# Optimization experiments

Hardware: AMD Instinct MI355X
Metric: run time of the kernel (lower is better)

## Reference

```python
import jax, jax.numpy as jnp
import numpy as np

B, S, D, H, SE, DE, DFF = 4, 1024, 1024, 16, 77, 768, 4096


def _ln(x, g, b, eps=1e-5):
    mu = jnp.mean(x, axis=-1, keepdims=True)
    var = jnp.mean((x - mu) ** 2, axis=-1, keepdims=True)
    return (x - mu) * jax.lax.rsqrt(var + eps) * g + b


def _split_heads(x, heads):
    b, s, d = x.shape
    return x.reshape(b, s, heads, d // heads).transpose(0, 2, 1, 3)  # b h s hd


def _attn(q, k, v, heads):
    # memory_efficient_attention equivalent: softmax(q k^T * scale) v, per head
    q, k, v = _split_heads(q, heads), _split_heads(k, heads), _split_heads(v, heads)
    scale = q.shape[-1] ** -0.5
    scores = jnp.einsum('bhqd,bhkd->bhqk', q, k) * scale
    probs = jax.nn.softmax(scores, axis=-1)
    o = jnp.einsum('bhqk,bhkd->bhqd', probs, v)
    b, h, s, hd = o.shape
    return o.transpose(0, 2, 1, 3).reshape(b, s, h * hd)


def _geglu_ff(x, w1, b1, w2, b2):
    proj = x @ w1 + b1
    a, gate = jnp.split(proj, 2, axis=-1)
    return (a * jax.nn.gelu(gate)) @ w2 + b2


def _forward(h1, h2, enc, wq, wk, wv, wqc, wo, bo, ln1g, ln1b, ln2g, ln2b,
             w2q, w2k, w2v, w2o, b2o, wff1, bff1, wff2, bff2):
    # norm1
    n1 = _ln(h1, ln1g[0], ln1b[0])
    n2 = _ln(h2, ln1g[1], ln1b[1])
    # dual-stream uni-direction attention (self + cross with swapped K/V)
    q1, k1, v1, q1c = n1 @ wq[0], n1 @ wk[0], n1 @ wv[0], n1 @ wqc[0]
    q2, k2, v2, q2c = n2 @ wq[1], n2 @ wk[1], n2 @ wv[1], n2 @ wqc[1]
    a1 = _attn(q1, k1, v1, H) + _attn(q1c, k2, v2, H)
    a2 = _attn(q2, k2, v2, H) + _attn(q2c, k1, v1, H)
    a1 = a1 @ wo[0] + bo[0]
    a2 = a2 @ wo[1] + bo[1]
    h1 = h1 + a1
    h2 = h2 + a2
    # cross attention to encoder states (attn2)
    n1 = _ln(h1, ln2g[0], ln2b[0])
    n2 = _ln(h2, ln2g[1], ln2b[1])
    c1 = _attn(n1 @ w2q[0], enc @ w2k[0], enc @ w2v[0], H) @ w2o[0] + b2o[0]
    c2 = _attn(n2 @ w2q[1], enc @ w2k[1], enc @ w2v[1], H) @ w2o[1] + b2o[1]
    h1 = h1 + c1
    h2 = h2 + c2
    # feed-forward (GEGLU), applied to norm2 output exactly as in source
    h1 = h1 + _geglu_ff(n1, wff1[0], bff1[0], wff2[0], bff2[0])
    h2 = h2 + _geglu_ff(n2, wff1[1], bff1[1], wff2[1], bff2[1])
    return (h1, h2)


def setup_inputs() -> dict:
    key = jax.random.key(0)
    ks = jax.random.split(key, 16)
    f = lambda k, shp: jax.random.normal(k, shp, jnp.float32) * 0.02
    return {
        'h1': jax.random.normal(ks[0], (B, S, D), jnp.float32),
        'h2': jax.random.normal(ks[1], (B, S, D), jnp.float32),
        'enc': jax.random.normal(ks[2], (B, SE, DE), jnp.float32),
        'wq': f(ks[3], (2, D, D)), 'wk': f(ks[4], (2, D, D)),
        'wv': f(ks[5], (2, D, D)), 'wqc': f(ks[6], (2, D, D)),
        'wo': f(ks[7], (2, D, D)), 'bo': jnp.zeros((2, D), jnp.float32),
        'ln1g': jnp.ones((2, D), jnp.float32), 'ln1b': jnp.zeros((2, D), jnp.float32),
        'ln2g': jnp.ones((2, D), jnp.float32), 'ln2b': jnp.zeros((2, D), jnp.float32),
        'w2q': f(ks[8], (2, D, D)), 'w2k': f(ks[9], (2, DE, D)),
        'w2v': f(ks[10], (2, DE, D)), 'w2o': f(ks[11], (2, D, D)),
        'b2o': jnp.zeros((2, D), jnp.float32),
        'wff1': f(ks[12], (2, D, 2 * DFF)), 'bff1': jnp.zeros((2, 2 * DFF), jnp.float32),
        'wff2': f(ks[13], (2, DFF, D)), 'bff2': jnp.zeros((2, D), jnp.float32),
    }


def reference(h1, h2, enc, wq, wk, wv, wqc, wo, bo, ln1g, ln1b, ln2g, ln2b,
              w2q, w2k, w2v, w2o, b2o, wff1, bff1, wff2, bff2):
    return _forward(h1, h2, enc, wq, wk, wv, wqc, wo, bo, ln1g, ln1b, ln2g, ln2b,
                    w2q, w2k, w2v, w2o, b2o, wff1, bff1, wff2, bff2)
```

## Files before the change

kernel.cpp:

```cpp
#include <hip/hip_runtime.h>

typedef unsigned short u16;
typedef short v8s __attribute__((ext_vector_type(8)));
typedef float v4f __attribute__((ext_vector_type(4)));

__device__ __forceinline__ float bf2f(u16 u) {
  union { unsigned u; float f; } c; c.u = ((unsigned)u) << 16; return c.f;
}
__device__ __forceinline__ u16 f2bf(float x) {
  union { float f; unsigned u; } c; c.f = x;
  unsigned r = c.u + 0x7fffu + ((c.u >> 16) & 1u);
  return (u16)(r >> 16);
}
__device__ __forceinline__ v4f vzero() { v4f z; z[0]=0.f; z[1]=0.f; z[2]=0.f; z[3]=0.f; return z; }
__device__ __forceinline__ v4f mfma16(v8s a, v8s b, v4f c) {
  return __builtin_amdgcn_mfma_f32_16x16x32_bf16(a, b, c, 0, 0, 0);
}
__device__ __forceinline__ void async_lds16(const void* g, void* l) {
  __builtin_amdgcn_global_load_lds((__attribute__((address_space(1))) void*)g,
                                   (__attribute__((address_space(3))) void*)l, 16, 0, 0);
}
__device__ __forceinline__ float gelu_f(float x) {
  return 0.5f * x * (1.f + tanhf(0.7978845608028654f * (x + 0.044715f * x * x * x)));
}

__global__ void detect_k(const unsigned* __restrict__ p, unsigned* __restrict__ flag) {
  if (threadIdx.x == 0) {
    flag[0] = (p[0] == 0x3F803F80u) ? 1u : 0u;
    flag[1] = 0u;
  }
}

__global__ __launch_bounds__(256) void cvt_k(const unsigned* __restrict__ flag,
    const void* __restrict__ src, u16* __restrict__ dst, int n) {
  int i = (blockIdx.x * 256 + threadIdx.x) * 8;
  if (i >= n) return;
  if (*flag) {
    *(uint4*)(dst + i) = *(const uint4*)((const u16*)src + i);
  } else {
    const float* s = (const float*)src + i;
    #pragma unroll
    for (int j = 0; j < 8; ++j) dst[i + j] = f2bf(s[j]);
  }
}

__global__ __launch_bounds__(256) void tr_k(const unsigned* __restrict__ flag,
    const void* __restrict__ in, u16* __restrict__ out, int R, int C, long outZS) {
  __shared__ u16 tile[32][33];
  size_t zin = (size_t)blockIdx.z * R * C;
  size_t zout = (size_t)blockIdx.z * outZS;
  int c0 = blockIdx.x * 32, r0 = blockIdx.y * 32;
  int tx = threadIdx.x & 31, ty = threadIdx.x >> 5;
  unsigned isbf = *flag;
  const u16* inb = (const u16*)in + zin;
  const float* inf = (const float*)in + zin;
  #pragma unroll
  for (int i = ty; i < 32; i += 8) {
    size_t idx = (size_t)(r0 + i) * C + c0 + tx;
    tile[i][tx] = isbf ? inb[idx] : f2bf(inf[idx]);
  }
  __syncthreads();
  out += zout;
  #pragma unroll
  for (int i = ty; i < 32; i += 8) out[(size_t)(c0 + i) * R + r0 + tx] = tile[tx][i];
}

__global__ __launch_bounds__(256) void vtr_k(const u16* __restrict__ in, u16* __restrict__ out) {
  __shared__ u16 tile[32][33];
  int z = blockIdx.z >> 2, b = blockIdx.z & 3;
  const u16* ip = in + (size_t)z * 16777216 + (size_t)b * 4194304 + 2048;
  u16* op = out + (size_t)z * 4194304 + (size_t)b * 1048576;
  int k0 = blockIdx.x * 32, d0 = blockIdx.y * 32;
  int tx = threadIdx.x & 31, ty = threadIdx.x >> 5;
  #pragma unroll
  for (int i = ty; i < 32; i += 8)
    tile[i][tx] = ip[(size_t)(k0 + i) * 4096 + d0 + tx];
  __syncthreads();
  #pragma unroll
  for (int i = ty; i < 32; i += 8)
    op[(size_t)(d0 + i) * 1024 + k0 + tx] = tile[tx][i];
}

__global__ __launch_bounds__(256) void ln_k(const unsigned* __restrict__ flag,
    const void* __restrict__ src0, const void* __restrict__ src1,
    const u16* __restrict__ gw, const u16* __restrict__ bw, u16* __restrict__ out) {
  int z = blockIdx.y;
  const void* src = z ? src1 : src0;
  out += (size_t)z * 4194304; gw += z * 1024; bw += z * 1024;
  int row = blockIdx.x, t = threadIdx.x;
  unsigned isbf = *flag;
  float4 v;
  if (isbf) {
    uint2 d = ((const uint2*)((const u16*)src + (size_t)row * 1024))[t];
    v.x = bf2f((u16)(d.x & 0xffffu)); v.y = bf2f((u16)(d.x >> 16));
    v.z = bf2f((u16)(d.y & 0xffffu)); v.w = bf2f((u16)(d.y >> 16));
  } else {
    v = ((const float4*)((const float*)src + (size_t)row * 1024))[t];
  }
  float s = v.x + v.y + v.z + v.w;
  float s2 = v.x * v.x + v.y * v.y + v.z * v.z + v.w * v.w;
  #pragma unroll
  for (int o = 32; o; o >>= 1) { s += __shfl_down(s, o); s2 += __shfl_down(s2, o); }
  __shared__ float red[8];
  int w = t >> 6;
  if ((t & 63) == 0) { red[w] = s; red[4 + w] = s2; }
  __syncthreads();
  if (t == 0) {
    red[0] = red[0] + red[1] + red[2] + red[3];
    red[4] = red[4] + red[5] + red[6] + red[7];
  }
  __syncthreads();
  float mu = red[0] * (1.f / 1024.f);
  float var = red[4] * (1.f / 1024.f) - mu * mu;
  float rstd = rsqrtf(var + 1e-5f);
  int c = t * 4;
  float xs[4] = { v.x, v.y, v.z, v.w };
  #pragma unroll
  for (int j = 0; j < 4; ++j) {
    float g = bf2f(gw[c + j]), bb = bf2f(bw[c + j]);
    out[(size_t)row * 1024 + c + j] = f2bf((xs[j] - mu) * rstd * g + bb);
  }
}

template<int EPI>
__global__ __launch_bounds__(256, 2) void gemm_bt(
    const u16* __restrict__ A, const u16* __restrict__ Bt,
    int M, int N, int K, int lda, int ldb, int ldc,
    const u16* __restrict__ bias, const u16* aux,
    float* __restrict__ resF, void* __restrict__ outB,
    long zsA, long zsB, long zsC, int zsBias,
    const void* rin0, const void* rin1,
    const unsigned* __restrict__ flagp)
{
  int z = blockIdx.z;
  A += (size_t)z * zsA;
  Bt += (size_t)z * zsB;
  size_t zc = (size_t)z * zsC;
  unsigned isbf = 0;
  if (EPI == 4 || EPI == 5) isbf = *flagp;
  const void* rin = (EPI == 5) ? (z ? rin1 : rin0) : nullptr;
  __shared__ alignas(16) u16 As[128 * 64];
  __shared__ alignas(16) u16 Bs[128 * 64];
  int tid = threadIdx.x;
  int lane = tid & 63, wave = tid >> 6;
  int l15 = lane & 15, l4 = lane >> 4;
  int wm = wave & 1, wn = wave >> 1;
  int m0 = blockIdx.x * 128, n0 = blockIdx.y * 128;
  v4f acc[4][4];
  #pragma unroll
  for (int i = 0; i < 4; ++i)
    #pragma unroll
    for (int j = 0; j < 4; ++j) acc[i][j] = vzero();

  for (int k0 = 0; k0 < K; k0 += 64) {
    #pragma unroll
    for (int it = 0; it < 4; ++it) {
      int sidx = it * 256 + tid;
      int r = sidx >> 3, cs = (sidx & 7) * 8;
      int ra = m0 + r; if (ra > M - 1) ra = M - 1;
      async_lds16(A + (size_t)ra * lda + k0 + cs, As + (size_t)(it * 256 + wave * 64) * 8);
      async_lds16(Bt + (size_t)(n0 + r) * ldb + k0 + cs, Bs + (size_t)(it * 256 + wave * 64) * 8);
    }
    __syncthreads();
    #pragma unroll
    for (int ks = 0; ks < 2; ++ks) {
      v8s af[4], bfr[4];
      #pragma unroll
      for (int i = 0; i < 4; ++i) {
        af[i]  = *(const v8s*)(As + (wm * 64 + i * 16 + l15) * 64 + ks * 32 + l4 * 8);
        bfr[i] = *(const v8s*)(Bs + (wn * 64 + i * 16 + l15) * 64 + ks * 32 + l4 * 8);
      }
      #pragma unroll
      for (int i = 0; i < 4; ++i)
        #pragma unroll
        for (int j = 0; j < 4; ++j)
          acc[i][j] = mfma16(af[i], bfr[j], acc[i][j]);
    }
    __syncthreads();
  }
  #pragma unroll
  for (int mt = 0; mt < 4; ++mt) {
    #pragma unroll
    for (int r = 0; r < 4; ++r) {
      int gr = m0 + wm * 64 + mt * 16 + l4 * 4 + r;
      if (gr >= M) continue;
      size_t ri = (size_t)gr * ldc;
      size_t ro = zc + ri;
      #pragma unroll
      for (int nt = 0; nt < 4; ++nt) {
        int gc = n0 + wn * 64 + nt * 16 + l15;
        float v = acc[mt][nt][r];
        if (bias) v += bf2f(bias[(size_t)z * zsBias + gc]);
        if (EPI == 0) ((u16*)outB)[ro + gc] = f2bf(v);
        else if (EPI == 1) ((u16*)outB)[ro + gc] = f2bf(gelu_f(v));
        else if (EPI == 2) ((u16*)outB)[ro + gc] = f2bf(v * bf2f(aux[ro + gc]));
        else if (EPI == 3) resF[ro + gc] += v;
        else if (EPI == 5) {
          float h = isbf ? bf2f(((const u16*)rin)[ri + gc]) : ((const float*)rin)[ri + gc];
          resF[ro + gc] = h + v;
        } else {
          float o = resF[ro + gc] + v;
          if (isbf) ((u16*)outB)[ro + gc] = f2bf(o);
          else ((float*)outB)[ro + gc] = o;
        }
      }
    }
  }
}

template<int EPI>
__global__ __launch_bounds__(512, 2) void gemm256(
    const u16* __restrict__ A, const u16* __restrict__ Bt,
    int M, int N, int K, int lda, int ldb, int ldc,
    const u16* __restrict__ bias, const u16* aux, void* __restrict__ outB,
    long zsA, long zsB, long zsC, int zsBias)
{
  __shared__ alignas(16) u16 As[4][8192];
  __shared__ alignas(16) u16 Bs[4][8192];
  int z = blockIdx.z;
  A += (size_t)z * zsA;
  Bt += (size_t)z * zsB;
  size_t zc = (size_t)z * zsC;
  int tid = threadIdx.x, lane = tid & 63, wave = tid >> 6;
  int l15 = lane & 15, l4 = lane >> 4;
  int wm = wave >> 2, wn = wave & 3;
  int m0 = blockIdx.x * 256, n0 = blockIdx.y * 256;
  int sa = l4 ^ ((l15 >> 1) & 3);
  int nG = K >> 5;

  v4f acc[8][4];
  #pragma unroll
  for (int i = 0; i < 8; ++i)
    #pragma unroll
    for (int j = 0; j < 4; ++j) acc[i][j] = vzero();

  auto stageA = [&](int g) {
    int sl = g & 3;
    #pragma unroll
    for (int l = 0; l < 2; ++l) {
      int sidx = l * 512 + tid;
      int r = sidx >> 2, c = sidx & 3;
      async_lds16(A + (size_t)(m0 + r) * lda + g * 32 + ((c ^ ((sidx >> 3) & 3)) * 8),
                  As[sl] + (size_t)(l * 512 + wave * 64) * 8);
    }
  };
  auto stageB = [&](int g) {
    int sl = g & 3;
    #pragma unroll
    for (int l = 0; l < 2; ++l) {
      int sidx = l * 512 + tid;
      int r = sidx >> 2, c = sidx & 3;
      async_lds16(Bt + (size_t)(n0 + r) * ldb + g * 32 + ((c ^ ((sidx >> 3) & 3)) * 8),
                  Bs[sl] + (size_t)(l * 512 + wave * 64) * 8);
    }
  };
  auto gate = [&](int cnt) {
    if (cnt >= 2)      asm volatile("s_waitcnt vmcnt(8)" ::: "memory");
    else if (cnt == 1) asm volatile("s_waitcnt vmcnt(4)" ::: "memory");
    else               asm volatile("s_waitcnt vmcnt(0)" ::: "memory");
    __builtin_amdgcn_sched_barrier(0);
  };

  stageA(0); stageB(0);
  if (1 < nG) { stageA(1); stageB(1); }
  if (2 < nG) { stageA(2); stageB(2); }
  gate((1 < nG) + (2 < nG));
  __builtin_amdgcn_s_barrier();

  auto kstep = [&](int t, int s0, int s1) {
    int g0 = 2 * t, g1 = 2 * t + 1;
    const u16* a0 = As[s0]; const u16* b0 = Bs[s0];
    const u16* a1 = As[s1]; const u16* b1 = Bs[s1];
    v8s af[4], bf[4];
    #pragma unroll
    for (int i = 0; i < 4; ++i) {
      af[i] = *(const v8s*)(a0 + ((wm * 128 + i * 16 + l15) * 4 + sa) * 8);
      bf[i] = *(const v8s*)(b0 + ((wn * 64 + i * 16 + l15) * 4 + sa) * 8);
    }
    if (g0 + 3 < nG) stageA(g0 + 3);
    __builtin_amdgcn_s_barrier();
    __builtin_amdgcn_s_setprio(1);
    #pragma unroll
    for (int i = 0; i < 4; ++i)
      #pragma unroll
      for (int j = 0; j < 4; ++j) acc[i][j] = mfma16(af[i], bf[j], acc[i][j]);
    __builtin_amdgcn_s_setprio(0);
    __builtin_amdgcn_s_barrier();
    #pragma unroll
    for (int i = 0; i < 4; ++i)
      af[i] = *(const v8s*)(a0 + ((wm * 128 + 64 + i * 16 + l15) * 4 + sa) * 8);
    if (g0 + 3 < nG) stageB(g0 + 3);
    __builtin_amdgcn_s_barrier();
    __builtin_amdgcn_s_setprio(1);
    #pragma unroll
    for (int i = 0; i < 4; ++i)
      #pragma unroll
      for (int j = 0; j < 4; ++j) acc[4 + i][j] = mfma16(af[i], bf[j], acc[4 + i][j]);
    __builtin_amdgcn_s_setprio(0);
    gate((g0 + 2 < nG) + (g0 + 3 < nG));
    __builtin_amdgcn_s_barrier();
    #pragma unroll
    for (int i = 0; i < 4; ++i) {
      af[i] = *(const v8s*)(a1 + ((wm * 128 + i * 16 + l15) * 4 + sa) * 8);
      bf[i] = *(const v8s*)(b1 + ((wn * 64 + i * 16 + l15) * 4 + sa) * 8);
    }
    if (g1 + 3 < nG) stageA(g1 + 3);
    __builtin_amdgcn_s_barrier();
    __builtin_amdgcn_s_setprio(1);
    #pragma unroll
    for (int i = 0; i < 4; ++i)
      #pragma unroll
      for (int j = 0; j < 4; ++j) acc[i][j] = mfma16(af[i], bf[j], acc[i][j]);
    __builtin_amdgcn_s_setprio(0);
    __builtin_amdgcn_s_barrier();
    #pragma unroll
    for (int i = 0; i < 4; ++i)
      af[i] = *(const v8s*)(a1 + ((wm * 128 + 64 + i * 16 + l15) * 4 + sa) * 8);
    if (g1 + 3 < nG) stageB(g1 + 3);
    __builtin_amdgcn_s_barrier();
    __builtin_amdgcn_s_setprio(1);
    #pragma unroll
    for (int i = 0; i < 4; ++i)
      #pragma unroll
      for (int j = 0; j < 4; ++j) acc[4 + i][j] = mfma16(af[i], bf[j], acc[4 + i][j]);
    __builtin_amdgcn_s_setprio(0);
    gate((g1 + 2 < nG) + (g1 + 3 < nG));
    __builtin_amdgcn_s_barrier();
  };

  int Ksteps = K >> 6;
  for (int t = 0; t < Ksteps; t += 2) {
    kstep(t, 0, 1);
    kstep(t + 1, 2, 3);
  }

  #pragma unroll
  for (int mi = 0; mi < 8; ++mi) {
    #pragma unroll
    for (int rr = 0; rr < 4; ++rr) {
      int gr = m0 + wm * 128 + mi * 16 + l4 * 4 + rr;
      size_t ro = zc + (size_t)gr * ldc;
      #pragma unroll
      for (int ni = 0; ni < 4; ++ni) {
        int gc = n0 + wn * 64 + ni * 16 + l15;
        float v = acc[mi][ni][rr];
        if (bias) v += bf2f(bias[(size_t)z * zsBias + gc]);
        if (EPI == 0) ((u16*)outB)[ro + gc] = f2bf(v);
        else if (EPI == 1) ((u16*)outB)[ro + gc] = f2bf(gelu_f(v));
        else ((u16*)outB)[ro + gc] = f2bf(v * bf2f(aux[ro + gc]));
      }
    }
  }
}

__global__ __launch_bounds__(256, 2) void flash_self_k(
    const u16* __restrict__ qkv, const u16* __restrict__ Vt, u16* __restrict__ O)
{
  __shared__ alignas(16) u16 Ksh[128 * 64];
  __shared__ alignas(16) u16 Vsh[64 * 128];
  __shared__ alignas(16) u16 Psh[4][16 * 128];
  int tid = threadIdx.x, lane = tid & 63, wave = tid >> 6;
  int l15 = lane & 15, l4 = lane >> 4;
  int h = blockIdx.y;
  int strm = blockIdx.z >> 2, b = blockIdx.z & 3;
  const size_t ZS = 16777216;
  const size_t BS = 4194304;
  int q0 = blockIdx.x * 64 + wave * 16;
  u16* pw = Psh[wave];
  int swz = l15 & 7;
  v4f res[4];
  #pragma unroll
  for (int i = 0; i < 4; ++i) res[i] = vzero();

  for (int sg = 0; sg < 2; ++sg) {
    int qcol = sg ? 3072 : 0;
    int ksrc = sg ? (strm ^ 1) : strm;
    const u16* Qb = qkv + (size_t)strm * ZS + (size_t)b * BS + qcol + h * 64;
    const u16* Kb = qkv + (size_t)ksrc * ZS + (size_t)b * BS + 1024 + h * 64;
    const u16* Vb = Vt + (size_t)ksrc * BS + (size_t)b * 1048576 + h * 65536;
    v8s qf0 = *(const v8s*)(Qb + (size_t)(q0 + l15) * 4096 + l4 * 8);
    v8s qf1 = *(const v8s*)(Qb + (size_t)(q0 + l15) * 4096 + l4 * 8 + 32);
    v4f oacc[4];
    #pragma unroll
    for (int i = 0; i < 4; ++i) oacc[i] = vzero();
    float mrun[4], lrun[4];
    #pragma unroll
    for (int r = 0; r < 4; ++r) { mrun[r] = -1e30f; lrun[r] = 0.f; }

    for (int c0 = 0; c0 < 1024; c0 += 128) {
      #pragma unroll
      for (int it = 0; it < 4; ++it) {
        int sidx = it * 256 + tid;
        int r = sidx >> 3, c = sidx & 7;
        async_lds16(Kb + (size_t)(c0 + r) * 4096 + ((c ^ (r & 7)) * 8),
                    Ksh + (size_t)(it * 256 + wave * 64) * 8);
      }
      #pragma unroll
      for (int it = 0; it < 4; ++it) {
        int sidx = it * 256 + tid;
        int d = sidx >> 4, c = sidx & 15;
        async_lds16(Vb + (size_t)d * 1024 + c0 + ((c ^ (d & 15)) * 8),
                    Vsh + (size_t)(it * 256 + wave * 64) * 8);
      }
      __syncthreads();
      v4f s[4][2];
      #pragma unroll
      for (int g = 0; g < 4; ++g) { s[g][0] = vzero(); s[g][1] = vzero(); }
      __builtin_amdgcn_s_setprio(1);
      #pragma unroll
      for (int g = 0; g < 4; ++g) {
        int rb0 = (g * 32 + l15) * 64, rb1 = rb0 + 16 * 64;
        v8s k00 = *(const v8s*)(Ksh + rb0 + ((l4 ^ swz) * 8));
        v8s k10 = *(const v8s*)(Ksh + rb1 + ((l4 ^ swz) * 8));
        v8s k01 = *(const v8s*)(Ksh + rb0 + (((4 + l4) ^ swz) * 8));
        v8s k11 = *(const v8s*)(Ksh + rb1 + (((4 + l4) ^ swz) * 8));
        s[g][0] = mfma16(qf0, k00, s[g][0]);
        s[g][1] = mfma16(qf0, k10, s[g][1]);
        s[g][0] = mfma16(qf1, k01, s[g][0]);
        s[g][1] = mfma16(qf1, k11, s[g][1]);
      }
      __builtin_amdgcn_s_setprio(0);
      float alpha[4];
      #pragma unroll
      for (int r = 0; r < 4; ++r) {
        int row = l4 * 4 + r;
        float x[8];
        #pragma unroll
        for (int g = 0; g < 4; ++g) {
          x[2 * g]     = s[g][0][r] * 0.125f;
          x[2 * g + 1] = s[g][1][r] * 0.125f;
        }
        float tm = fmaxf(fmaxf(fmaxf(x[0], x[1]), fmaxf(x[2], x[3])),
                         fmaxf(fmaxf(x[4], x[5]), fmaxf(x[6], x[7])));
        #pragma unroll
        for (int o = 8; o; o >>= 1) tm = fmaxf(tm, __shfl_xor(tm, o));
        float mn = fmaxf(mrun[r], tm);
        alpha[r] = __expf(mrun[r] - mn);
        mrun[r] = mn;
        float rs = 0.f;
        #pragma unroll
        for (int j = 0; j < 8; ++j) {
          float p = __expf(x[j] - mn);
          rs += p;
          int col = (j >> 1) * 32 + (j & 1) * 16 + l15;
          pw[row * 128 + (((col >> 3) ^ row) * 8) + (col & 7)] = f2bf(p);
        }
        #pragma unroll
        for (int o = 8; o; o >>= 1) rs += __shfl_xor(rs, o);
        lrun[r] = lrun[r] * alpha[r] + rs;
      }
      #pragma unroll
      for (int nt = 0; nt < 4; ++nt)
        #pragma unroll
        for (int r = 0; r < 4; ++r) oacc[nt][r] *= alpha[r];
      __builtin_amdgcn_s_setprio(1);
      #pragma unroll
      for (int g = 0; g < 4; ++g) {
        v8s pa = *(const v8s*)(pw + l15 * 128 + (((g * 4 + l4) ^ l15) * 8));
        #pragma unroll
        for (int nt = 0; nt < 4; ++nt) {
          int vr = nt * 16 + l15;
          v8s vb = *(const v8s*)(Vsh + vr * 128 + (((g * 4 + l4) ^ (vr & 15)) * 8));
          oacc[nt] = mfma16(pa, vb, oacc[nt]);
        }
      }
      __builtin_amdgcn_s_setprio(0);
      __syncthreads();
    }
    #pragma unroll
    for (int r = 0; r < 4; ++r) {
      float inv = 1.f / lrun[r];
      #pragma unroll
      for (int nt = 0; nt < 4; ++nt) res[nt][r] += oacc[nt][r] * inv;
    }
  }
  #pragma unroll
  for (int nt = 0; nt < 4; ++nt) {
    #pragma unroll
    for (int r = 0; r < 4; ++r) {
      int gq = q0 + l4 * 4 + r;
      size_t oi = (size_t)strm * BS + ((size_t)b * 1024 + gq) * 1024 + h * 64 + nt * 16 + l15;
      O[oi] = f2bf(res[nt][r]);
    }
  }
}

__global__ __launch_bounds__(256, 2) void flash_cross_k(
    const u16* __restrict__ Q, const u16* __restrict__ KV, u16* __restrict__ O)
{
  __shared__ alignas(16) u16 Ksh[128 * 64];
  __shared__ alignas(16) unsigned VshT[64 * 68];
  __shared__ alignas(16) u16 Psh[4][16 * 128];
  int tid = threadIdx.x, lane = tid & 63, wave = tid >> 6;
  int l15 = lane & 15, l4 = lane >> 4;
  int h = blockIdx.y;
  int strm = blockIdx.z >> 2, b = blockIdx.z & 3;
  const u16* Qb = Q + (size_t)strm * 4194304 + (size_t)b * 1048576 + h * 64;
  const u16* Kb = KV + (size_t)strm * 630784 + (size_t)b * 157696 + h * 64;
  const u16* Vb = Kb + 1024;
  int q0 = blockIdx.x * 64 + wave * 16;
  u16* pw = Psh[wave];
  int swz = l15 & 7;
  v8s qf0 = *(const v8s*)(Qb + (size_t)(q0 + l15) * 1024 + l4 * 8);
  v8s qf1 = *(const v8s*)(Qb + (size_t)(q0 + l15) * 1024 + l4 * 8 + 32);

  #pragma unroll
  for (int it = 0; it < 4; ++it) {
    int sidx = it * 256 + tid;
    int r = sidx >> 3, c = sidx & 7;
    int gk = r > 76 ? 76 : r;
    async_lds16(Kb + (size_t)gk * 2048 + ((c ^ (r & 7)) * 8),
                Ksh + (size_t)(it * 256 + wave * 64) * 8);
  }
  #pragma unroll
  for (int it = 0; it < 2; ++it) {
    int tt = it * 256 + tid;
    int kp = tt & 63, dsg = tt >> 6;
    int gk0 = kp * 2, gk1 = kp * 2 + 1;
    if (gk0 > 76) gk0 = 76;
    if (gk1 > 76) gk1 = 76;
    v8s v0 = *(const v8s*)(Vb + (size_t)gk0 * 2048 + dsg * 8);
    v8s v1 = *(const v8s*)(Vb + (size_t)gk1 * 2048 + dsg * 8);
    #pragma unroll
    for (int j = 0; j < 8; ++j) {
      unsigned pk = (unsigned)(u16)v0[j] | ((unsigned)(u16)v1[j] << 16);
      VshT[(dsg * 8 + j) * 68 + kp] = pk;
    }
  }
  __syncthreads();
  v4f s[4][2];
  #pragma unroll
  for (int g = 0; g < 4; ++g) { s[g][0] = vzero(); s[g][1] = vzero(); }
  __builtin_amdgcn_s_setprio(1);
  #pragma unroll
  for (int g = 0; g < 4; ++g) {
    int rb0 = (g * 32 + l15) * 64, rb1 = rb0 + 16 * 64;
    v8s k00 = *(const v8s*)(Ksh + rb0 + ((l4 ^ swz) * 8));
    v8s k10 = *(const v8s*)(Ksh + rb1 + ((l4 ^ swz) * 8));
    v8s k01 = *(const v8s*)(Ksh + rb0 + (((4 + l4) ^ swz) * 8));
    v8s k11 = *(const v8s*)(Ksh + rb1 + (((4 + l4) ^ swz) * 8));
    s[g][0] = mfma16(qf0, k00, s[g][0]);
    s[g][1] = mfma16(qf0, k10, s[g][1]);
    s[g][0] = mfma16(qf1, k01, s[g][0]);
    s[g][1] = mfma16(qf1, k11, s[g][1]);
  }
  __builtin_amdgcn_s_setprio(0);
  float lsum[4];
  #pragma unroll
  for (int r = 0; r < 4; ++r) {
    int row = l4 * 4 + r;
    float x[8];
    #pragma unroll
    for (int g = 0; g < 4; ++g) {
      bool ok0 = (g * 32 + l15) < 77, ok1 = (g * 32 + 16 + l15) < 77;
      x[2 * g]     = ok0 ? s[g][0][r] * 0.125f : -1e30f;
      x[2 * g + 1] = ok1 ? s[g][1][r] * 0.125f : -1e30f;
    }
    float tm = fmaxf(fmaxf(fmaxf(x[0], x[1]), fmaxf(x[2], x[3])),
                     fmaxf(fmaxf(x[4], x[5]), fmaxf(x[6], x[7])));
    #pragma unroll
    for (int o = 8; o; o >>= 1) tm = fmaxf(tm, __shfl_xor(tm, o));
    float rs = 0.f;
    #pragma unroll
    for (int j = 0; j < 8; ++j) {
      float p = __expf(x[j] - tm);
      rs += p;
      int col = (j >> 1) * 32 + (j & 1) * 16 + l15;
      pw[row * 128 + (((col >> 3) ^ row) * 8) + (col & 7)] = f2bf(p);
    }
    #pragma unroll
    for (int o = 8; o; o >>= 1) rs += __shfl_xor(rs, o);
    lsum[r] = rs;
  }
  v4f oacc[4];
  #pragma unroll
  for (int i = 0; i < 4; ++i) oacc[i] = vzero();
  __builtin_amdgcn_s_setprio(1);
  #pragma unroll
  for (int g = 0; g < 4; ++g) {
    v8s pa = *(const v8s*)(pw + l15 * 128 + (((g * 4 + l4) ^ l15) * 8));
    #pragma unroll
    for (int nt = 0; nt < 4; ++nt) {
      v8s vb = *(const v8s*)((const u16*)VshT + (nt * 16 + l15) * 136 + g * 32 + l4 * 8);
      oacc[nt] = mfma16(pa, vb, oacc[nt]);
    }
  }
  __builtin_amdgcn_s_setprio(0);
  #pragma unroll
  for (int nt = 0; nt < 4; ++nt) {
    #pragma unroll
    for (int r = 0; r < 4; ++r) {
      int gq = q0 + l4 * 4 + r;
      size_t oi = (size_t)strm * 4194304 + ((size_t)b * 1024 + gq) * 1024 + h * 64 + nt * 16 + l15;
      O[oi] = f2bf(oacc[nt][r] / lsum[r]);
    }
  }
}

extern "C" void kernel_launch(void* const* d_in, const int* in_sizes, int n_in,
                              void* d_out, int out_size, void* d_ws, size_t ws_size,
                              hipStream_t stream)
{
  (void)in_sizes; (void)n_in; (void)out_size;
  const void* h1   = d_in[0];
  const void* h2   = d_in[1];
  const void* enc  = d_in[2];
  const void* wq   = d_in[3];
  const void* wk   = d_in[4];
  const void* wv   = d_in[5];
  const void* wqc  = d_in[6];
  const void* wo   = d_in[7];
  const void* bo   = d_in[8];
  const void* ln1g = d_in[9];
  const void* ln1b = d_in[10];
  const void* ln2g = d_in[11];
  const void* ln2b = d_in[12];
  const void* w2q  = d_in[13];
  const void* w2k  = d_in[14];
  const void* w2v  = d_in[15];
  const void* w2o  = d_in[16];
  const void* b2o  = d_in[17];
  const void* wff1 = d_in[18];
  const void* bff1 = d_in[19];
  const void* wff2 = d_in[20];
  const void* bff2 = d_in[21];

  const size_t S1 = 4194304;
  const size_t W1 = 1048576;
  const size_t QS = 16777216;
  const size_t NE = 236544;

  char* base = (char*)d_ws;
  size_t off = 0;
  auto AL = [&](size_t n) { size_t r = off; off += (n + 255) & ~(size_t)255; return r; };
  size_t o_flag   = AL(256);
  size_t o_pb     = AL(30720 * 2);
  size_t o_encB   = AL(NE * 2);
  size_t o_wqkvT  = AL(2 * 4 * W1 * 2);
  size_t o_woT    = AL(2 * W1 * 2);
  size_t o_w2qT   = AL(2 * W1 * 2);
  size_t o_w2oT   = AL(2 * W1 * 2);
  size_t o_w2kvT  = AL(2 * 2048 * 768 * 2);
  size_t o_wff1T  = AL(2 * 8192 * 1024 * 2);
  size_t o_wff2T  = AL(2 * 4096 * 1024 * 2);
  size_t o_hw     = AL(2 * S1 * 4);
  size_t o_n      = AL(2 * S1 * 2);
  size_t o_qkv    = AL(2 * QS * 2);
  size_t o_ab     = AL(2 * S1 * 2);
  if (ws_size < off) return;

  unsigned* flagp = (unsigned*)(base + o_flag);
  const unsigned* zerop = flagp + 1;
  u16* pb = (u16*)(base + o_pb);
  u16* boB   = pb + 0;
  u16* b2oB  = pb + 2048;
  u16* ln1gB = pb + 4096;
  u16* ln1bB = pb + 6144;
  u16* ln2gB = pb + 8192;
  u16* ln2bB = pb + 10240;
  u16* bff2B = pb + 12288;
  u16* bff1B = pb + 14336;
  u16* encB  = (u16*)(base + o_encB);
  u16* wqkvT = (u16*)(base + o_wqkvT);
  u16* woT   = (u16*)(base + o_woT);
  u16* w2qT  = (u16*)(base + o_w2qT);
  u16* w2oT  = (u16*)(base + o_w2oT);
  u16* w2kvT = (u16*)(base + o_w2kvT);
  u16* wff1T = (u16*)(base + o_wff1T);
  u16* wff2T = (u16*)(base + o_wff2T);
  float* hw  = (float*)(base + o_hw);
  u16* n1    = (u16*)(base + o_n);
  u16* qkv   = (u16*)(base + o_qkv);
  u16* a1b   = (u16*)(base + o_ab);
  u16* q1x   = qkv;
  u16* c1b   = qkv + 2 * S1;
  u16* kencv = qkv + 4 * S1;
  u16* gelu  = qkv;
  u16* vtb   = n1;

  auto tr = [&](const void* ip, u16* op, int R, int C, long outZS) {
    dim3 g(C / 32, R / 32, 2);
    tr_k<<<g, 256, 0, stream>>>(flagp, ip, op, R, C, outZS);
  };
  auto cvt = [&](const void* ip, u16* op, int n) {
    cvt_k<<<(n / 8 + 255) / 256, 256, 0, stream>>>(flagp, ip, op, n);
  };
  auto gemm = [&](int epi, const u16* Ap, const u16* Bp, int M, int N, int K,
                  int lda, int ldb, int ldc, const u16* bias, const u16* aux,
                  float* resF, void* oB, int nz, long zsA, long zsB, long zsC, int zsBias,
                  const void* rin0, const void* rin1) {
    dim3 g((M + 127) / 128, N / 128, nz);
    switch (epi) {
      case 0: gemm_bt<0><<<g, 256, 0, stream>>>(Ap, Bp, M, N, K, lda, ldb, ldc, bias, aux, resF, oB, zsA, zsB, zsC, zsBias, rin0, rin1, flagp); break;
      case 1: gemm_bt<1><<<g, 256, 0, stream>>>(Ap, Bp, M, N, K, lda, ldb, ldc, bias, aux, resF, oB, zsA, zsB, zsC, zsBias, rin0, rin1, flagp); break;
      case 2: gemm_bt<2><<<g, 256, 0, stream>>>(Ap, Bp, M, N, K, lda, ldb, ldc, bias, aux, resF, oB, zsA, zsB, zsC, zsBias, rin0, rin1, flagp); break;
      case 3: gemm_bt<3><<<g, 256, 0, stream>>>(Ap, Bp, M, N, K, lda, ldb, ldc, bias, aux, resF, oB, zsA, zsB, zsC, zsBias, rin0, rin1, flagp); break;
      case 4: gemm_bt<4><<<g, 256, 0, stream>>>(Ap, Bp, M, N, K, lda, ldb, ldc, bias, aux, resF, oB, zsA, zsB, zsC, zsBias, rin0, rin1, flagp); break;
      default: gemm_bt<5><<<g, 256, 0, stream>>>(Ap, Bp, M, N, K, lda, ldb, ldc, bias, aux, resF, oB, zsA, zsB, zsC, zsBias, rin0, rin1, flagp); break;
    }
  };

  detect_k<<<1, 64, 0, stream>>>((const unsigned*)ln1g, flagp);
  cvt(bo, boB, 2048);     cvt(b2o, b2oB, 2048);
  cvt(ln1g, ln1gB, 2048); cvt(ln1b, ln1bB, 2048);
  cvt(ln2g, ln2gB, 2048); cvt(ln2b, ln2bB, 2048);
  cvt(bff2, bff2B, 2048); cvt(bff1, bff1B, 16384);
  cvt(enc, encB, (int)NE);
  tr(wq,  wqkvT + 0 * W1, 1024, 1024, 4 * (long)W1);
  tr(wk,  wqkvT + 1 * W1, 1024, 1024, 4 * (long)W1);
  tr(wv,  wqkvT + 2 * W1, 1024, 1024, 4 * (long)W1);
  tr(wqc, wqkvT + 3 * W1, 1024, 1024, 4 * (long)W1);
  tr(wo,  woT,  1024, 1024, (long)W1);
  tr(w2q, w2qT, 1024, 1024, (long)W1);
  tr(w2o, w2oT, 1024, 1024, (long)W1);
  tr(w2k, w2kvT + 0,          768, 1024, 2048L * 768);
  tr(w2v, w2kvT + 1024 * 768, 768, 1024, 2048L * 768);
  tr(wff1, wff1T, 1024, 8192, 8192L * 1024);
  tr(wff2, wff2T, 4096, 1024, 4096L * 1024);
  ln_k<<<dim3(4096, 2), 256, 0, stream>>>(flagp, h1, h2, ln1gB, ln1bB, n1);
  gemm256<0><<<dim3(16, 16, 2), 512, 0, stream>>>(n1, wqkvT, 4096, 4096, 1024,
      1024, 1024, 4096, nullptr, nullptr, qkv, (long)S1, 4 * (long)W1, (long)QS, 0);
  vtr_k<<<dim3(32, 32, 8), 256, 0, stream>>>(qkv, vtb);
  flash_self_k<<<dim3(16, 16, 8), 256, 0, stream>>>(qkv, vtb, a1b);
  gemm(5, a1b, woT, 4096, 1024, 1024, 1024, 1024, 1024, boB, nullptr, hw, nullptr,
       2, (long)S1, (long)W1, (long)S1, 1024, h1, h2);
  ln_k<<<dim3(4096, 2), 256, 0, stream>>>(zerop, hw, hw + S1, ln2gB, ln2bB, n1);
  gemm(0, n1, w2qT, 4096, 1024, 1024, 1024, 1024, 1024, nullptr, nullptr, nullptr, q1x,
       2, (long)S1, (long)W1, (long)S1, 0, nullptr, nullptr);
  gemm(0, encB, w2kvT, 308, 2048, 768, 768, 768, 2048, nullptr, nullptr, nullptr, kencv,
       2, 0, 2048L * 768, 308L * 2048, 0, nullptr, nullptr);
  flash_cross_k<<<dim3(16, 16, 8), 256, 0, stream>>>(q1x, kencv, c1b);
  gemm(3, c1b, w2oT, 4096, 1024, 1024, 1024, 1024, 1024, b2oB, nullptr, hw, nullptr,
       2, (long)S1, (long)W1, (long)S1, 1024, nullptr, nullptr);
  gemm256<1><<<dim3(16, 16, 2), 512, 0, stream>>>(n1, wff1T + 4096 * 1024, 4096, 4096, 1024,
      1024, 1024, 4096, bff1B + 4096, nullptr, gelu, (long)S1, 8192L * 1024, (long)QS, 8192);
  gemm256<2><<<dim3(16, 16, 2), 512, 0, stream>>>(n1, wff1T, 4096, 4096, 1024,
      1024, 1024, 4096, bff1B, gelu, gelu, (long)S1, 8192L * 1024, (long)QS, 8192);
  gemm(4, gelu, wff2T, 4096, 1024, 4096, 4096, 4096, 1024,
       bff2B, nullptr, hw, d_out, 2, (long)QS, 4096L * 1024, (long)S1, 1024,
       nullptr, nullptr);
}
```

Measured before the change: 1.199 ms.

## Keep softmax probabilities in registers, skip rescales, swizzle block order

The self-attention kernel now computes S transposed (K as the A operand), so each lane owns one query's scores. That lets it pack the probabilities to bf16 in registers with v_cvt_pk_bf16_f32 and feed them straight into the PV MFMA, removing the per-wave LDS P buffer and its round trip. Online-softmax max rescaling is skipped unless the max grows by more than a threshold, and occupancy is raised to 4 blocks per CU. Both GEMMs and the flash kernel also remap block indices for L2 locality, and the V transpose permutes key columns to match the new P register layout. These changes cut LDS traffic, shuffles and exp work, at the cost of subtle layout coupling and higher register pressure.

```diff
diff --git a/kernel.cpp b/kernel.cpp
--- a/kernel.cpp
+++ b/kernel.cpp
@@ -19,6 +19,11 @@
 __device__ __forceinline__ void async_lds16(const void* g, void* l) {
   __builtin_amdgcn_global_load_lds((__attribute__((address_space(1))) void*)g,
                                    (__attribute__((address_space(3))) void*)l, 16, 0, 0);
+}
+__device__ __forceinline__ unsigned cvtpk(float lo, float hi) {
+  unsigned r;
+  asm("v_cvt_pk_bf16_f32 %0, %1, %2" : "=v"(r) : "v"(lo), "v"(hi));
+  return r;
 }
 __device__ __forceinline__ float gelu_f(float x) {
   return 0.5f * x * (1.f + tanhf(0.7978845608028654f * (x + 0.044715f * x * x * x)));
@@ -76,9 +81,10 @@
   for (int i = ty; i < 32; i += 8)
     tile[i][tx] = ip[(size_t)(k0 + i) * 4096 + d0 + tx];
   __syncthreads();
+  int sl = (((tx >> 3) & 1) << 4) | (((tx >> 2) & 1) << 3) | (((tx >> 4) & 1) << 2) | (tx & 3);
   #pragma unroll
   for (int i = ty; i < 32; i += 8)
-    op[(size_t)(d0 + i) * 1024 + k0 + tx] = tile[tx][i];
+    op[(size_t)(d0 + i) * 1024 + k0 + sl] = tile[tx][i];
 }
 
 __global__ __launch_bounds__(256) void ln_k(const unsigned* __restrict__ flag,
@@ -145,7 +151,11 @@
   int lane = tid & 63, wave = tid >> 6;
   int l15 = lane & 15, l4 = lane >> 4;
   int wm = wave & 1, wn = wave >> 1;
-  int m0 = blockIdx.x * 128, n0 = blockIdx.y * 128;
+  int lin = blockIdx.x + blockIdx.y * gridDim.x;
+  int nxy = gridDim.x * gridDim.y;
+  int sw = (lin & 7) * (nxy >> 3) + (lin >> 3);
+  int bx = sw % gridDim.x, by = sw / gridDim.x;
+  int m0 = bx * 128, n0 = by * 128;
   v4f acc[4][4];
   #pragma unroll
   for (int i = 0; i < 4; ++i)
@@ -224,7 +234,11 @@
   int tid = threadIdx.x, lane = tid & 63, wave = tid >> 6;
   int l15 = lane & 15, l4 = lane >> 4;
   int wm = wave >> 2, wn = wave & 3;
-  int m0 = blockIdx.x * 256, n0 = blockIdx.y * 256;
+  int lin = blockIdx.x + blockIdx.y * gridDim.x;
+  int nxy = gridDim.x * gridDim.y;
+  int sw = (lin & 7) * (nxy >> 3) + (lin >> 3);
+  int bx = sw % gridDim.x, by = sw / gridDim.x;
+  int m0 = bx * 256, n0 = by * 256;
   int sa = l4 ^ ((l15 >> 1) & 3);
   int nG = K >> 5;
 
@@ -353,20 +367,20 @@
   }
 }
 
-__global__ __launch_bounds__(256, 2) void flash_self_k(
+__global__ __launch_bounds__(256, 4) void flash_self_k(
     const u16* __restrict__ qkv, const u16* __restrict__ Vt, u16* __restrict__ O)
 {
   __shared__ alignas(16) u16 Ksh[128 * 64];
   __shared__ alignas(16) u16 Vsh[64 * 128];
-  __shared__ alignas(16) u16 Psh[4][16 * 128];
   int tid = threadIdx.x, lane = tid & 63, wave = tid >> 6;
-  int l15 = lane & 15, l4 = lane >> 4;
-  int h = blockIdx.y;
-  int strm = blockIdx.z >> 2, b = blockIdx.z & 3;
+  int l15 = lane & 15, l4 = (lane >> 4) & 3;
+  int lin = blockIdx.x + (blockIdx.y << 4) + (blockIdx.z << 8);
+  int sw = (lin & 7) * 256 + (lin >> 3);
+  int qblk = sw & 15, h = (sw >> 4) & 15, zb = sw >> 8;
+  int strm = zb >> 2, b = zb & 3;
   const size_t ZS = 16777216;
   const size_t BS = 4194304;
-  int q0 = blockIdx.x * 64 + wave * 16;
-  u16* pw = Psh[wave];
+  int q0 = qblk * 64 + wave * 16;
   int swz = l15 & 7;
   v4f res[4];
   #pragma unroll
@@ -383,9 +397,7 @@
     v4f oacc[4];
     #pragma unroll
     for (int i = 0; i < 4; ++i) oacc[i] = vzero();
-    float mrun[4], lrun[4];
-    #pragma unroll
-    for (int r = 0; r < 4; ++r) { mrun[r] = -1e30f; lrun[r] = 0.f; }
+    float mrun = -1e30f, lrun = 0.f;
 
     for (int c0 = 0; c0 < 1024; c0 += 128) {
       #pragma unroll
@@ -414,54 +426,63 @@
         v8s k10 = *(const v8s*)(Ksh + rb1 + ((l4 ^ swz) * 8));
         v8s k01 = *(const v8s*)(Ksh + rb0 + (((4 + l4) ^ swz) * 8));
         v8s k11 = *(const v8s*)(Ksh + rb1 + (((4 + l4) ^ swz) * 8));
-        s[g][0] = mfma16(qf0, k00, s[g][0]);
-        s[g][1] = mfma16(qf0, k10, s[g][1]);
-        s[g][0] = mfma16(qf1, k01, s[g][0]);
-        s[g][1] = mfma16(qf1, k11, s[g][1]);
+        s[g][0] = mfma16(k00, qf0, s[g][0]);
+        s[g][1] = mfma16(k10, qf0, s[g][1]);
+        s[g][0] = mfma16(k01, qf1, s[g][0]);
+        s[g][1] = mfma16(k11, qf1, s[g][1]);
       }
       __builtin_amdgcn_s_setprio(0);
-      float alpha[4];
-      #pragma unroll
-      for (int r = 0; r < 4; ++r) {
-        int row = l4 * 4 + r;
-        float x[8];
+      float tm = -1e30f;
+      #pragma unroll
+      for (int g = 0; g < 4; ++g)
         #pragma unroll
-        for (int g = 0; g < 4; ++g) {
-          x[2 * g]     = s[g][0][r] * 0.125f;
-          x[2 * g + 1] = s[g][1][r] * 0.125f;
+        for (int hh = 0; hh < 2; ++hh)
+          #pragma unroll
+          for (int r = 0; r < 4; ++r) {
+            s[g][hh][r] *= 0.125f;
+            tm = fmaxf(tm, s[g][hh][r]);
+          }
+      tm = fmaxf(tm, __shfl_xor(tm, 16));
+      tm = fmaxf(tm, __shfl_xor(tm, 32));
+      float alpha = 1.f;
+      if (!__all(tm <= mrun + 8.f)) {
+        float mn = fmaxf(mrun, tm);
+        alpha = __expf(mrun - mn);
+        mrun = mn;
+        #pragma unroll
+        for (int r = 0; r < 4; ++r) {
+          float ar = __shfl(alpha, l4 * 4 + r);
+          #pragma unroll
+          for (int nt = 0; nt < 4; ++nt) oacc[nt][r] *= ar;
         }
-        float tm = fmaxf(fmaxf(fmaxf(x[0], x[1]), fmaxf(x[2], x[3])),
-                         fmaxf(fmaxf(x[4], x[5]), fmaxf(x[6], x[7])));
+      }
+      float rs = 0.f;
+      unsigned pk[4][4];
+      #pragma unroll
+      for (int g = 0; g < 4; ++g)
         #pragma unroll
-        for (int o = 8; o; o >>= 1) tm = fmaxf(tm, __shfl_xor(tm, o));
-        float mn = fmaxf(mrun[r], tm);
-        alpha[r] = __expf(mrun[r] - mn);
-        mrun[r] = mn;
-        float rs = 0.f;
-        #pragma unroll
-        for (int j = 0; j < 8; ++j) {
-          float p = __expf(x[j] - mn);
-          rs += p;
-          int col = (j >> 1) * 32 + (j & 1) * 16 + l15;
-          pw[row * 128 + (((col >> 3) ^ row) * 8) + (col & 7)] = f2bf(p);
+        for (int hh = 0; hh < 2; ++hh) {
+          float p0 = __expf(s[g][hh][0] - mrun);
+          float p1 = __expf(s[g][hh][1] - mrun);
+          float p2 = __expf(s[g][hh][2] - mrun);
+          float p3 = __expf(s[g][hh][3] - mrun);
+          rs += (p0 + p1) + (p2 + p3);
+          pk[g][hh * 2]     = cvtpk(p0, p1);
+          pk[g][hh * 2 + 1] = cvtpk(p2, p3);
         }
-        #pragma unroll
-        for (int o = 8; o; o >>= 1) rs += __shfl_xor(rs, o);
-        lrun[r] = lrun[r] * alpha[r] + rs;
-      }
-      #pragma unroll
-      for (int nt = 0; nt < 4; ++nt)
-        #pragma unroll
-        for (int r = 0; r < 4; ++r) oacc[nt][r] *= alpha[r];
+      rs += __shfl_xor(rs, 16);
+      rs += __shfl_xor(rs, 32);
+      lrun = lrun * alpha + rs;
       __builtin_amdgcn_s_setprio(1);
       #pragma unroll
       for (int g = 0; g < 4; ++g) {
-        v8s pa = *(const v8s*)(pw + l15 * 128 + (((g * 4 + l4) ^ l15) * 8));
+        union { unsigned u[4]; v8s v; } pa;
+        pa.u[0] = pk[g][0]; pa.u[1] = pk[g][1]; pa.u[2] = pk[g][2]; pa.u[3] = pk[g][3];
         #pragma unroll
         for (int nt = 0; nt < 4; ++nt) {
           int vr = nt * 16 + l15;
           v8s vb = *(const v8s*)(Vsh + vr * 128 + (((g * 4 + l4) ^ (vr & 15)) * 8));
-          oacc[nt] = mfma16(pa, vb, oacc[nt]);
+          oacc[nt] = mfma16(pa.v, vb, oacc[nt]);
         }
       }
       __builtin_amdgcn_s_setprio(0);
@@ -469,7 +490,8 @@
     }
     #pragma unroll
     for (int r = 0; r < 4; ++r) {
-      float inv = 1.f / lrun[r];
+      float lr = __shfl(lrun, l4 * 4 + r);
+      float inv = 1.f / lr;
       #pragma unroll
       for (int nt = 0; nt < 4; ++nt) res[nt][r] += oacc[nt][r] * inv;
     }
```

Measured after the change: 1.133 ms. 5.5% less time.
